# Optimization experiments

Measured on AMD Instinct MI355X. Metric: run time of the kernel, lower is better.

The kernel has to match this reference:

```python
import jax, jax.numpy as jnp
import numpy as np

VOCAB, EMBED, HID, LAYERS, OUT = 50000, 256, 256, 2, 50
B, S = 64, 512
H = HID // 2  # per-direction hidden size


def setup_inputs() -> dict:
    key = jax.random.key(0)
    ks = jax.random.split(key, 12)
    sc = 0.05
    embed = jax.random.normal(ks[0], (VOCAB, EMBED), jnp.float32) * sc
    embed = embed.at[1].set(0.0)  # padding_idx=1
    return {
        "x": jax.random.randint(ks[1], (B, S), 0, VOCAB),
        "embed": embed,
        "W1": jax.random.normal(ks[2], (HID, EMBED), jnp.float32) * sc,
        "b1": jax.random.normal(ks[3], (HID,), jnp.float32) * sc,
        "gru_Wih": jax.random.normal(ks[4], (LAYERS, 2, 3 * H, HID), jnp.float32) * sc,
        "gru_Whh": jax.random.normal(ks[5], (LAYERS, 2, 3 * H, H), jnp.float32) * sc,
        "gru_bih": jax.random.normal(ks[6], (LAYERS, 2, 3 * H), jnp.float32) * sc,
        "gru_bhh": jax.random.normal(ks[7], (LAYERS, 2, 3 * H), jnp.float32) * sc,
        "W2": jax.random.normal(ks[8], (HID, HID), jnp.float32) * sc,
        "b2": jax.random.normal(ks[9], (HID,), jnp.float32) * sc,
        "W3": jax.random.normal(ks[10], (OUT, HID), jnp.float32) * sc,
        "b3": jax.random.normal(ks[11], (OUT,), jnp.float32) * sc,
    }


def _gru_dir(x, Wih, Whh, bih, bhh, reverse):
    # x: [B, S, D]; PyTorch gate order: r, z, n. h0 = zeros.
    xp = jnp.einsum("bsd,gd->bsg", x, Wih) + bih  # [B, S, 3H], input proj hoisted out of scan
    xs = jnp.swapaxes(xp, 0, 1)  # [S, B, 3H]
    h0 = jnp.zeros((x.shape[0], Whh.shape[1]), x.dtype)

    def step(h, xt):
        hp = h @ Whh.T + bhh  # [B, 3H]
        xr, xz, xn = jnp.split(xt, 3, axis=-1)
        hr, hz, hn = jnp.split(hp, 3, axis=-1)
        r = jax.nn.sigmoid(xr + hr)
        z = jax.nn.sigmoid(xz + hz)
        n = jnp.tanh(xn + r * hn)
        h_new = (1.0 - z) * n + z * h
        return h_new, h_new

    _, ys = jax.lax.scan(step, h0, xs, reverse=reverse)  # outputs kept in original time order
    return jnp.swapaxes(ys, 0, 1)  # [B, S, H]


def reference(x, embed, W1, b1, gru_Wih, gru_Whh, gru_bih, gru_bhh, W2, b2, W3, b3):
    h = embed[x]  # [B, S, E]
    h = h @ W1.T + b1  # [B, S, HID]
    for l in range(gru_Wih.shape[0]):
        out_f = _gru_dir(h, gru_Wih[l, 0], gru_Whh[l, 0], gru_bih[l, 0], gru_bhh[l, 0], False)
        out_b = _gru_dir(h, gru_Wih[l, 1], gru_Whh[l, 1], gru_bih[l, 1], gru_bhh[l, 1], True)
        h = jnp.concatenate([out_f, out_b], axis=-1) + h  # bidirectional concat + residual
    h = jax.nn.gelu(h @ W2.T + b2, approximate=False)  # nn.GELU default is exact erf
    return h @ W3.T + b3  # [B, S, OUT]
```

## Files before the change

kernel.cpp:

```cpp
#include <hip/hip_runtime.h>

typedef unsigned int uint;
typedef unsigned short ushort;

typedef __attribute__((ext_vector_type(8))) short sh8;
typedef __attribute__((ext_vector_type(4))) float f32x4;

__device__ __forceinline__ ushort f2b(float f) {
    uint x = __float_as_uint(f);
    x += 0x7fffu + ((x >> 16) & 1u);
    return (ushort)(x >> 16);
}
__device__ __forceinline__ float b2f(ushort u) {
    return __uint_as_float(((uint)u) << 16);
}
__device__ __forceinline__ uint pack2(float a, float b) {
    return (uint)f2b(a) | ((uint)f2b(b) << 16);
}
__device__ __forceinline__ uint cvt_pk_bf16(float lo, float hi) {
    uint r;
    asm("v_cvt_pk_bf16_f32 %0, %1, %2" : "=v"(r) : "v"(lo), "v"(hi));
    return r;
}
__device__ __forceinline__ float frcp(float x) { return __builtin_amdgcn_rcpf(x); }
__device__ __forceinline__ float sigmf(float x) { return frcp(1.0f + __expf(-x)); }
__device__ __forceinline__ float tanhf2(float y) {
    return fmaf(2.0f, frcp(1.0f + __expf(-2.0f * y)), -1.0f);
}

__global__ __launch_bounds__(256) void k_detx(const uint* __restrict__ xw,
                                              int* __restrict__ flag) {
    __shared__ int sh[256];
    int t = threadIdx.x;
    int c = 0;
    for (int i = t; i < 2048; i += 256) c += (xw[2 * i + 1] == 0u) ? 1 : 0;
    sh[t] = c;
    __syncthreads();
    if (t == 0) {
        int s = 0;
        for (int i = 0; i < 256; i++) s += sh[i];
        flag[0] = (s >= 1843) ? 1 : 0;
    }
}

__global__ __launch_bounds__(256) void k_gather(const void* __restrict__ x,
                                                const float* __restrict__ embed,
                                                const int* __restrict__ flag,
                                                ushort* __restrict__ out) {
    int chunk = blockIdx.x * 256 + threadIdx.x;
    int row = chunk >> 5;
    int c = chunk & 31;
    int v;
    if (flag[0]) {
        v = (int)((const uint*)x)[2 * row];
    } else {
        v = ((const int*)x)[row];
    }
    v = min(max(v, 0), 49999);
    const float4* e = (const float4*)&embed[(size_t)v * 256 + (size_t)c * 8];
    float4 a = e[0], b = e[1];
    uint4 pv;
    pv.x = pack2(a.x, a.y);
    pv.y = pack2(a.z, a.w);
    pv.z = pack2(b.x, b.y);
    pv.w = pack2(b.z, b.w);
    *(uint4*)&out[(size_t)row * 256 + (size_t)c * 8] = pv;
}

__global__ __launch_bounds__(256) void k_gemm_bt(const ushort* __restrict__ A,
                                                 const float* __restrict__ Wf,
                                                 const float* __restrict__ bias,
                                                 ushort* __restrict__ Cb,
                                                 float* __restrict__ Cf,
                                                 int M, int N, int K, int gelu) {
    __shared__ __align__(16) ushort Al[128 * 32];
    __shared__ __align__(16) ushort Bl[128 * 32];
    int tid = threadIdx.x;
    int bm = blockIdx.x, bn = blockIdx.y;
    int wid = tid >> 6, lane = tid & 63;
    int ln = lane & 15, kq = lane >> 4;
    int wm = (wid & 1) * 64, wn = (wid >> 1) * 64;
    int rowA0 = bm * 128, rowB0 = bn * 128;

    f32x4 acc[4][4];
#pragma unroll
    for (int i = 0; i < 4; i++)
#pragma unroll
        for (int j = 0; j < 4; j++) acc[i][j] = (f32x4){0.f, 0.f, 0.f, 0.f};

    for (int kt = 0; kt < K; kt += 32) {
#pragma unroll
        for (int c = tid; c < 512; c += 256) {
            int r = c >> 2, c8 = (c & 3) * 8;
            *(uint4*)&Al[r * 32 + c8] =
                *(const uint4*)&A[(size_t)(rowA0 + r) * K + kt + c8];
            int nb = rowB0 + r;
            uint4 bv = {0u, 0u, 0u, 0u};
            if (nb < N) {
                const float4* wp = (const float4*)&Wf[(size_t)nb * K + kt + c8];
                float4 w0 = wp[0], w1 = wp[1];
                bv.x = pack2(w0.x, w0.y);
                bv.y = pack2(w0.z, w0.w);
                bv.z = pack2(w1.x, w1.y);
                bv.w = pack2(w1.z, w1.w);
            }
            *(uint4*)&Bl[r * 32 + c8] = bv;
        }
        __syncthreads();
        sh8 af[4], bfr[4];
#pragma unroll
        for (int i = 0; i < 4; i++)
            af[i] = *(const sh8*)&Al[(wm + i * 16 + ln) * 32 + kq * 8];
#pragma unroll
        for (int j = 0; j < 4; j++)
            bfr[j] = *(const sh8*)&Bl[(wn + j * 16 + ln) * 32 + kq * 8];
#pragma unroll
        for (int i = 0; i < 4; i++)
#pragma unroll
            for (int j = 0; j < 4; j++)
                acc[i][j] = __builtin_amdgcn_mfma_f32_16x16x32_bf16(
                    af[i], bfr[j], acc[i][j], 0, 0, 0);
        __syncthreads();
    }

#pragma unroll
    for (int i = 0; i < 4; i++)
#pragma unroll
        for (int j = 0; j < 4; j++) {
            int col = rowB0 + wn + j * 16 + ln;
            if (col >= N) continue;
            float bv = bias[col];
#pragma unroll
            for (int reg = 0; reg < 4; reg++) {
                int row = rowA0 + wm + i * 16 + kq * 4 + reg;
                float v = acc[i][j][reg] + bv;
                if (gelu) v = 0.5f * v * (1.0f + erff(v * 0.70710678118f));
                if (Cb) Cb[(size_t)row * N + col] = f2b(v);
                if (Cf) Cf[(size_t)row * N + col] = v;
            }
        }
}

struct PF {
    uint xr, xz, xn, rv;
};

#define GLOAD(dst, off, base, IMM)                                            \
    asm volatile("global_load_ushort %0, %1, %2 offset:" IMM                  \
                 : "=v"(dst)                                                  \
                 : "v"(off), "s"(base))

#define GSTORE(off, data, base)                                               \
    asm volatile("global_store_short %0, %1, %2" ::"v"(off), "v"(data),       \
                 "s"(base))

#define PREF(p)                                                               \
    {                                                                         \
        GLOAD(p.xr, xo_ld, xp, "0");                                          \
        GLOAD(p.xz, xo_ld, xp, "256");                                        \
        GLOAD(p.xn, xo_ld, xp, "512");                                        \
        GLOAD(p.rv, ho_ld, hb, "0");                                          \
        xo_ld += XS;                                                          \
        ho_ld += HS;                                                          \
    }

#define GSTEP(PAR, p, WN, DP)                                                 \
    {                                                                         \
        asm volatile("s_waitcnt vmcnt(" #WN ")");                             \
        __builtin_amdgcn_sched_barrier(0);                                    \
        float xr = __uint_as_float(p.xr << 16);                               \
        float xz = __uint_as_float(p.xz << 16);                               \
        float xn = __uint_as_float(p.xn << 16);                               \
        float rv = __uint_as_float(p.rv << 16);                               \
        if (DP) {                                                             \
            PREF(p)                                                           \
        }                                                                     \
        const ushort* hrd = lds + (PAR)*576 + (ln & 3) * 144 + kq * 8;        \
        sh8 a0 = *(const sh8*)(hrd);                                          \
        sh8 a1 = *(const sh8*)(hrd + 32);                                     \
        sh8 a2 = *(const sh8*)(hrd + 64);                                     \
        sh8 a3 = *(const sh8*)(hrd + 96);                                     \
        f32x4 accr = (f32x4){0.f, 0.f, 0.f, 0.f};                             \
        f32x4 accz = accr, accn = accr;                                       \
        accr = __builtin_amdgcn_mfma_f32_16x16x32_bf16(a0, bfrag[0][0], accr, 0, 0, 0); \
        accz = __builtin_amdgcn_mfma_f32_16x16x32_bf16(a0, bfrag[1][0], accz, 0, 0, 0); \
        accn = __builtin_amdgcn_mfma_f32_16x16x32_bf16(a0, bfrag[2][0], accn, 0, 0, 0); \
        accr = __builtin_amdgcn_mfma_f32_16x16x32_bf16(a1, bfrag[0][1], accr, 0, 0, 0); \
        accz = __builtin_amdgcn_mfma_f32_16x16x32_bf16(a1, bfrag[1][1], accz, 0, 0, 0); \
        accn = __builtin_amdgcn_mfma_f32_16x16x32_bf16(a1, bfrag[2][1], accn, 0, 0, 0); \
        accr = __builtin_amdgcn_mfma_f32_16x16x32_bf16(a2, bfrag[0][2], accr, 0, 0, 0); \
        accz = __builtin_amdgcn_mfma_f32_16x16x32_bf16(a2, bfrag[1][2], accz, 0, 0, 0); \
        accn = __builtin_amdgcn_mfma_f32_16x16x32_bf16(a2, bfrag[2][2], accn, 0, 0, 0); \
        accr = __builtin_amdgcn_mfma_f32_16x16x32_bf16(a3, bfrag[0][3], accr, 0, 0, 0); \
        accz = __builtin_amdgcn_mfma_f32_16x16x32_bf16(a3, bfrag[1][3], accz, 0, 0, 0); \
        accn = __builtin_amdgcn_mfma_f32_16x16x32_bf16(a3, bfrag[2][3], accn, 0, 0, 0); \
        float ar = b2 ? (b1 ? accr[3] : accr[2]) : (b1 ? accr[1] : accr[0]);  \
        float az = b2 ? (b1 ? accz[3] : accz[2]) : (b1 ? accz[1] : accz[0]);  \
        float an = b2 ? (b1 ? accn[3] : accn[2]) : (b1 ? accn[1] : accn[0]);  \
        float rg = sigmf(xr + ar + bh_r);                                     \
        float zg = sigmf(xz + az + bh_z);                                     \
        float ng = tanhf2(fmaf(rg, an + bh_n, xn));                           \
        float h = fmaf(zg, hstate - ng, ng);                                  \
        hstate = h;                                                           \
        float sv = h + rv;                                                    \
        uint pk = cvt_pk_bf16(h, sv);                                         \
        lds[(1 - (PAR)) * 576 + ob * 144 + jcol] = (ushort)pk;                \
        uint svb = pk >> 16;                                                  \
        GSTORE(ho_st, svb, hb);                                               \
        ho_st += HS;                                                          \
        asm volatile("s_waitcnt lgkmcnt(0)");                                 \
        __builtin_amdgcn_sched_barrier(0);                                    \
        __builtin_amdgcn_s_barrier();                                         \
        __builtin_amdgcn_sched_barrier(0);                                    \
    }

template <int DS>
__device__ __forceinline__ void gru_impl(const ushort* __restrict__ xp,
                                         const float* __restrict__ Whh_l,
                                         const float* __restrict__ bhh_l,
                                         ushort* __restrict__ hb,
                                         int dir, int b_base, int t,
                                         ushort* lds) {
    constexpr int XS = DS * 1536;
    constexpr int HS = DS * 512;
    const int w = t >> 6, l = t & 63;
    const int ln = l & 15, kq = l >> 4;
    const int jcol = (w << 4) + ln;
    const int ob = kq;
    const bool b1 = (ob & 1) != 0, b2 = (ob & 2) != 0;

    const float* Wd = Whh_l + (size_t)dir * 384 * 128;
    const float* bhh_d = bhh_l + dir * 384;

    sh8 bfrag[3][4];
#pragma unroll
    for (int g = 0; g < 3; g++)
#pragma unroll
        for (int kt = 0; kt < 4; kt++) {
            const float4* wp =
                (const float4*)(Wd + (size_t)(g * 128 + jcol) * 128 + kt * 32 + kq * 8);
            float4 w0 = wp[0], w1 = wp[1];
            uint4 pv;
            pv.x = pack2(w0.x, w0.y);
            pv.y = pack2(w0.z, w0.w);
            pv.z = pack2(w1.x, w1.y);
            pv.w = pack2(w1.z, w1.w);
            bfrag[g][kt] = *(sh8*)&pv;
        }

    const float bh_r = bhh_d[jcol];
    const float bh_z = bhh_d[128 + jcol];
    const float bh_n = bhh_d[256 + jcol];
    asm volatile("" ::"v"(bh_r), "v"(bh_z), "v"(bh_n));

    const int t0 = (DS > 0) ? 0 : 511;
    int row0 = (b_base + ob) * 512 + t0;
    int xo_ld = row0 * 1536 + (dir * 384 + jcol) * 2;
    int ho_ld = row0 * 512 + (dir * 128 + jcol) * 2;
    int ho_st = ho_ld;

    float hstate = 0.f;

    for (int i = t; i < 2 * 576; i += 512) lds[i] = 0;
    __syncthreads();

    PF pA, pB;
    PREF(pA)
    PREF(pB)

    GSTEP(0, pA, 4, 1)
    GSTEP(1, pB, 5, 1)
    for (int s = 2; s < 510; s += 2) {
        GSTEP(0, pA, 6, 1)
        GSTEP(1, pB, 6, 1)
    }
    GSTEP(0, pA, 6, 0)
    GSTEP(1, pB, 2, 0)
}

__global__ __launch_bounds__(512, 1) void k_gru(const ushort* __restrict__ xp,
                                                const float* __restrict__ Whh_l,
                                                const float* __restrict__ bhh_l,
                                                ushort* __restrict__ hb) {
    __shared__ __align__(16) ushort lds[2 * 576];
    const int dir = blockIdx.x & 1;
    const int b_base = (blockIdx.x >> 1) << 2;
    if (dir == 0)
        gru_impl<1>(xp, Whh_l, bhh_l, hb, dir, b_base, threadIdx.x, lds);
    else
        gru_impl<-1>(xp, Whh_l, bhh_l, hb, dir, b_base, threadIdx.x, lds);
}

extern "C" void kernel_launch(void* const* d_in, const int* in_sizes, int n_in,
                              void* d_out, int out_size, void* d_ws, size_t ws_size,
                              hipStream_t stream) {
    const void* x = d_in[0];
    const float* embed = (const float*)d_in[1];
    const float* W1 = (const float*)d_in[2];
    const float* b1 = (const float*)d_in[3];
    const float* Wih = (const float*)d_in[4];
    const float* Whh = (const float*)d_in[5];
    const float* bih = (const float*)d_in[6];
    const float* bhh = (const float*)d_in[7];
    const float* W2 = (const float*)d_in[8];
    const float* b2 = (const float*)d_in[9];
    const float* W3 = (const float*)d_in[10];
    const float* b3 = (const float*)d_in[11];

    char* ws = (char*)d_ws;
    ushort* xp = (ushort*)ws;
    ushort* hb = (ushort*)(ws + 32768ull * 768 * 2);
    ushort* embA = xp;
    ushort* g = xp;
    int* xflag = (int*)hb;

    k_detx<<<1, 256, 0, stream>>>((const uint*)x, xflag);
    k_gather<<<4096, 256, 0, stream>>>(x, embed, xflag, embA);
    k_gemm_bt<<<dim3(256, 2), 256, 0, stream>>>(embA, W1, b1, hb, (float*)0,
                                                32768, 256, 256, 0);

    k_gemm_bt<<<dim3(256, 6), 256, 0, stream>>>(hb, Wih, bih, xp, (float*)0,
                                                32768, 768, 256, 0);
    k_gru<<<32, 512, 0, stream>>>(xp, Whh, bhh, hb);

    k_gemm_bt<<<dim3(256, 6), 256, 0, stream>>>(hb, Wih + 196608, bih + 768,
                                                xp, (float*)0, 32768, 768, 256, 0);
    k_gru<<<32, 512, 0, stream>>>(xp, Whh + 98304, bhh + 768, hb);

    k_gemm_bt<<<dim3(256, 2), 256, 0, stream>>>(hb, W2, b2, g, (float*)0,
                                                32768, 256, 256, 1);
    k_gemm_bt<<<dim3(256, 1), 256, 0, stream>>>(g, W3, b3, (ushort*)0,
                                                (float*)d_out, 32768, 50, 256, 0);
}
```

Baseline: 674.0 us.

## Halve GRU block to 4 waves, each computing two 16-column hidden tiles

The recurrent GRU kernel now runs with 256 threads (4 waves) per block instead of 512. Each wave owns 32 hidden columns and issues 24 MFMAs per step instead of 12, with doubled prefetch registers, bias values and weight fragments. The aim is to cut the per-step block barrier cost and wave synchronization on the serial critical path, at the price of longer per-wave MFMA chains and higher register pressure.

After: 810.2 us. 20.2% more time.

```diff
diff --git a/kernel.cpp b/kernel.cpp
--- a/kernel.cpp
+++ b/kernel.cpp
@@ -142,7 +142,8 @@
 }
 
 struct PF {
-    uint xr, xz, xn, rv;
+    uint xr0, xz0, xn0, rv0;
+    uint xr1, xz1, xn1, rv1;
 };
 
 #define GLOAD(dst, off, base, IMM)                                            \
@@ -150,28 +151,38 @@
                  : "=v"(dst)                                                  \
                  : "v"(off), "s"(base))
 
-#define GSTORE(off, data, base)                                               \
-    asm volatile("global_store_short %0, %1, %2" ::"v"(off), "v"(data),       \
-                 "s"(base))
+#define GSTORE(off, data, base, IMM)                                          \
+    asm volatile("global_store_short %0, %1, %2 offset:" IMM ::"v"(off),      \
+                 "v"(data), "s"(base))
 
 #define PREF(p)                                                               \
     {                                                                         \
-        GLOAD(p.xr, xo_ld, xp, "0");                                          \
-        GLOAD(p.xz, xo_ld, xp, "256");                                        \
-        GLOAD(p.xn, xo_ld, xp, "512");                                        \
-        GLOAD(p.rv, ho_ld, hb, "0");                                          \
+        GLOAD(p.xr0, xo_ld, xp, "0");                                         \
+        GLOAD(p.xz0, xo_ld, xp, "256");                                       \
+        GLOAD(p.xn0, xo_ld, xp, "512");                                       \
+        GLOAD(p.rv0, ho_ld, hb, "0");                                         \
+        GLOAD(p.xr1, xo_ld, xp, "32");                                        \
+        GLOAD(p.xz1, xo_ld, xp, "288");                                       \
+        GLOAD(p.xn1, xo_ld, xp, "544");                                       \
+        GLOAD(p.rv1, ho_ld, hb, "32");                                        \
         xo_ld += XS;                                                          \
         ho_ld += HS;                                                          \
     }
+
+#define SEL(v) (b2 ? (b1 ? (v)[3] : (v)[2]) : (b1 ? (v)[1] : (v)[0]))
 
 #define GSTEP(PAR, p, WN, DP)                                                 \
     {                                                                         \
         asm volatile("s_waitcnt vmcnt(" #WN ")");                             \
         __builtin_amdgcn_sched_barrier(0);                                    \
-        float xr = __uint_as_float(p.xr << 16);                               \
-        float xz = __uint_as_float(p.xz << 16);                               \
-        float xn = __uint_as_float(p.xn << 16);                               \
-        float rv = __uint_as_float(p.rv << 16);                               \
+        float xr0 = __uint_as_float(p.xr0 << 16);                             \
+        float xz0 = __uint_as_float(p.xz0 << 16);                             \
+        float xn0 = __uint_as_float(p.xn0 << 16);                             \
+        float rv0 = __uint_as_float(p.rv0 << 16);                             \
+        float xr1 = __uint_as_float(p.xr1 << 16);                             \
+        float xz1 = __uint_as_float(p.xz1 << 16);                             \
+        float xn1 = __uint_as_float(p.xn1 << 16);                             \
+        float rv1 = __uint_as_float(p.rv1 << 16);                             \
         if (DP) {                                                             \
             PREF(p)                                                           \
         }                                                                     \
@@ -180,33 +191,53 @@
         sh8 a1 = *(const sh8*)(hrd + 32);                                     \
         sh8 a2 = *(const sh8*)(hrd + 64);                                     \
         sh8 a3 = *(const sh8*)(hrd + 96);                                     \
-        f32x4 accr = (f32x4){0.f, 0.f, 0.f, 0.f};                             \
-        f32x4 accz = accr, accn = accr;                                       \
-        accr = __builtin_amdgcn_mfma_f32_16x16x32_bf16(a0, bfrag[0][0], accr, 0, 0, 0); \
-        accz = __builtin_amdgcn_mfma_f32_16x16x32_bf16(a0, bfrag[1][0], accz, 0, 0, 0); \
-        accn = __builtin_amdgcn_mfma_f32_16x16x32_bf16(a0, bfrag[2][0], accn, 0, 0, 0); \
-        accr = __builtin_amdgcn_mfma_f32_16x16x32_bf16(a1, bfrag[0][1], accr, 0, 0, 0); \
-        accz = __builtin_amdgcn_mfma_f32_16x16x32_bf16(a1, bfrag[1][1], accz, 0, 0, 0); \
-        accn = __builtin_amdgcn_mfma_f32_16x16x32_bf16(a1, bfrag[2][1], accn, 0, 0, 0); \
-        accr = __builtin_amdgcn_mfma_f32_16x16x32_bf16(a2, bfrag[0][2], accr, 0, 0, 0); \
-        accz = __builtin_amdgcn_mfma_f32_16x16x32_bf16(a2, bfrag[1][2], accz, 0, 0, 0); \
-        accn = __builtin_amdgcn_mfma_f32_16x16x32_bf16(a2, bfrag[2][2], accn, 0, 0, 0); \
-        accr = __builtin_amdgcn_mfma_f32_16x16x32_bf16(a3, bfrag[0][3], accr, 0, 0, 0); \
-        accz = __builtin_amdgcn_mfma_f32_16x16x32_bf16(a3, bfrag[1][3], accz, 0, 0, 0); \
-        accn = __builtin_amdgcn_mfma_f32_16x16x32_bf16(a3, bfrag[2][3], accn, 0, 0, 0); \
-        float ar = b2 ? (b1 ? accr[3] : accr[2]) : (b1 ? accr[1] : accr[0]);  \
-        float az = b2 ? (b1 ? accz[3] : accz[2]) : (b1 ? accz[1] : accz[0]);  \
-        float an = b2 ? (b1 ? accn[3] : accn[2]) : (b1 ? accn[1] : accn[0]);  \
-        float rg = sigmf(xr + ar + bh_r);                                     \
-        float zg = sigmf(xz + az + bh_z);                                     \
-        float ng = tanhf2(fmaf(rg, an + bh_n, xn));                           \
-        float h = fmaf(zg, hstate - ng, ng);                                  \
-        hstate = h;                                                           \
-        float sv = h + rv;                                                    \
-        uint pk = cvt_pk_bf16(h, sv);                                         \
-        lds[(1 - (PAR)) * 576 + ob * 144 + jcol] = (ushort)pk;                \
-        uint svb = pk >> 16;                                                  \
-        GSTORE(ho_st, svb, hb);                                               \
+        f32x4 ac[6];                                                          \
+        _Pragma("unroll") for (int q_ = 0; q_ < 6; q_++)                      \
+            ac[q_] = (f32x4){0.f, 0.f, 0.f, 0.f};                             \
+        ac[0] = __builtin_amdgcn_mfma_f32_16x16x32_bf16(a0, bfrag[0][0], ac[0], 0, 0, 0); \
+        ac[1] = __builtin_amdgcn_mfma_f32_16x16x32_bf16(a0, bfrag[1][0], ac[1], 0, 0, 0); \
+        ac[2] = __builtin_amdgcn_mfma_f32_16x16x32_bf16(a0, bfrag[2][0], ac[2], 0, 0, 0); \
+        ac[3] = __builtin_amdgcn_mfma_f32_16x16x32_bf16(a0, bfrag[3][0], ac[3], 0, 0, 0); \
+        ac[4] = __builtin_amdgcn_mfma_f32_16x16x32_bf16(a0, bfrag[4][0], ac[4], 0, 0, 0); \
+        ac[5] = __builtin_amdgcn_mfma_f32_16x16x32_bf16(a0, bfrag[5][0], ac[5], 0, 0, 0); \
+        ac[0] = __builtin_amdgcn_mfma_f32_16x16x32_bf16(a1, bfrag[0][1], ac[0], 0, 0, 0); \
+        ac[1] = __builtin_amdgcn_mfma_f32_16x16x32_bf16(a1, bfrag[1][1], ac[1], 0, 0, 0); \
+        ac[2] = __builtin_amdgcn_mfma_f32_16x16x32_bf16(a1, bfrag[2][1], ac[2], 0, 0, 0); \
+        ac[3] = __builtin_amdgcn_mfma_f32_16x16x32_bf16(a1, bfrag[3][1], ac[3], 0, 0, 0); \
+        ac[4] = __builtin_amdgcn_mfma_f32_16x16x32_bf16(a1, bfrag[4][1], ac[4], 0, 0, 0); \
+        ac[5] = __builtin_amdgcn_mfma_f32_16x16x32_bf16(a1, bfrag[5][1], ac[5], 0, 0, 0); \
+        ac[0] = __builtin_amdgcn_mfma_f32_16x16x32_bf16(a2, bfrag[0][2], ac[0], 0, 0, 0); \
+        ac[1] = __builtin_amdgcn_mfma_f32_16x16x32_bf16(a2, bfrag[1][2], ac[1], 0, 0, 0); \
+        ac[2] = __builtin_amdgcn_mfma_f32_16x16x32_bf16(a2, bfrag[2][2], ac[2], 0, 0, 0); \
+        ac[3] = __builtin_amdgcn_mfma_f32_16x16x32_bf16(a2, bfrag[3][2], ac[3], 0, 0, 0); \
+        ac[4] = __builtin_amdgcn_mfma_f32_16x16x32_bf16(a2, bfrag[4][2], ac[4], 0, 0, 0); \
+        ac[5] = __builtin_amdgcn_mfma_f32_16x16x32_bf16(a2, bfrag[5][2], ac[5], 0, 0, 0); \
+        ac[0] = __builtin_amdgcn_mfma_f32_16x16x32_bf16(a3, bfrag[0][3], ac[0], 0, 0, 0); \
+        ac[1] = __builtin_amdgcn_mfma_f32_16x16x32_bf16(a3, bfrag[1][3], ac[1], 0, 0, 0); \
+        ac[2] = __builtin_amdgcn_mfma_f32_16x16x32_bf16(a3, bfrag[2][3], ac[2], 0, 0, 0); \
+        ac[3] = __builtin_amdgcn_mfma_f32_16x16x32_bf16(a3, bfrag[3][3], ac[3], 0, 0, 0); \
+        ac[4] = __builtin_amdgcn_mfma_f32_16x16x32_bf16(a3, bfrag[4][3], ac[4], 0, 0, 0); \
+        ac[5] = __builtin_amdgcn_mfma_f32_16x16x32_bf16(a3, bfrag[5][3], ac[5], 0, 0, 0); \
+        float ar0 = SEL(ac[0]), az0 = SEL(ac[1]), an0 = SEL(ac[2]);           \
+        float ar1 = SEL(ac[3]), az1 = SEL(ac[4]), an1 = SEL(ac[5]);           \
+        float rg0 = sigmf(xr0 + ar0 + bh_r0);                                 \
+        float zg0 = sigmf(xz0 + az0 + bh_z0);                                 \
+        float ng0 = tanhf2(fmaf(rg0, an0 + bh_n0, xn0));                      \
+        float h0 = fmaf(zg0, hst0 - ng0, ng0);                                \
+        hst0 = h0;                                                            \
+        float rg1 = sigmf(xr1 + ar1 + bh_r1);                                 \
+        float zg1 = sigmf(xz1 + az1 + bh_z1);                                 \
+        float ng1 = tanhf2(fmaf(rg1, an1 + bh_n1, xn1));                      \
+        float h1 = fmaf(zg1, hst1 - ng1, ng1);                                \
+        hst1 = h1;                                                            \
+        uint pk0 = cvt_pk_bf16(h0, h0 + rv0);                                 \
+        uint pk1 = cvt_pk_bf16(h1, h1 + rv1);                                 \
+        ushort* hw = lds + (1 - (PAR)) * 576 + kq * 144 + wb + ln;            \
+        hw[0] = (ushort)pk0;                                                  \
+        hw[16] = (ushort)pk1;                                                 \
+        uint sv0 = pk0 >> 16, sv1 = pk1 >> 16;                                \
+        GSTORE(ho_st, sv0, hb, "0");                                          \
+        GSTORE(ho_st, sv1, hb, "32");                                         \
         ho_st += HS;                                                          \
         asm volatile("s_waitcnt lgkmcnt(0)");                                 \
         __builtin_amdgcn_sched_barrier(0);                                    \
@@ -225,60 +256,66 @@
     constexpr int HS = DS * 512;
     const int w = t >> 6, l = t & 63;
     const int ln = l & 15, kq = l >> 4;
-    const int jcol = (w << 4) + ln;
-    const int ob = kq;
-    const bool b1 = (ob & 1) != 0, b2 = (ob & 2) != 0;
+    const int wb = w * 32;
+    const bool b1 = (kq & 1) != 0, b2 = (kq & 2) != 0;
 
     const float* Wd = Whh_l + (size_t)dir * 384 * 128;
     const float* bhh_d = bhh_l + dir * 384;
 
-    sh8 bfrag[3][4];
+    sh8 bfrag[6][4];
 #pragma unroll
     for (int g = 0; g < 3; g++)
 #pragma unroll
-        for (int kt = 0; kt < 4; kt++) {
-            const float4* wp =
-                (const float4*)(Wd + (size_t)(g * 128 + jcol) * 128 + kt * 32 + kq * 8);
-            float4 w0 = wp[0], w1 = wp[1];
-            uint4 pv;
-            pv.x = pack2(w0.x, w0.y);
-            pv.y = pack2(w0.z, w0.w);
-            pv.z = pack2(w1.x, w1.y);
-            pv.w = pack2(w1.z, w1.w);
-            bfrag[g][kt] = *(sh8*)&pv;
-        }
-
-    const float bh_r = bhh_d[jcol];
-    const float bh_z = bhh_d[128 + jcol];
-    const float bh_n = bhh_d[256 + jcol];
-    asm volatile("" ::"v"(bh_r), "v"(bh_z), "v"(bh_n));
+        for (int c = 0; c < 2; c++)
+#pragma unroll
+            for (int kt = 0; kt < 4; kt++) {
+                const float4* wp = (const float4*)(
+                    Wd + (size_t)(g * 128 + wb + c * 16 + ln) * 128 + kt * 32 +
+                    kq * 8);
+                float4 w0 = wp[0], w1 = wp[1];
+                uint4 pv;
+                pv.x = pack2(w0.x, w0.y);
+                pv.y = pack2(w0.z, w0.w);
+                pv.z = pack2(w1.x, w1.y);
+                pv.w = pack2(w1.z, w1.w);
+                bfrag[c * 3 + g][kt] = *(sh8*)&pv;
+            }
+
+    const float bh_r0 = bhh_d[wb + ln];
+    const float bh_z0 = bhh_d[128 + wb + ln];
+    const float bh_n0 = bhh_d[256 + wb + ln];
+    const float bh_r1 = bhh_d[wb + 16 + ln];
+    const float bh_z1 = bhh_d[128 + wb + 16 + ln];
+    const float bh_n1 = bhh_d[256 + wb + 16 + ln];
+    asm volatile("" ::"v"(bh_r0), "v"(bh_z0), "v"(bh_n0), "v"(bh_r1),
+                 "v"(bh_z1), "v"(bh_n1));
 
     const int t0 = (DS > 0) ? 0 : 511;
-    int row0 = (b_base + ob) * 512 + t0;
-    int xo_ld = row0 * 1536 + (dir * 384 + jcol) * 2;
-    int ho_ld = row0 * 512 + (dir * 128 + jcol) * 2;
+    int row0 = (b_base + kq) * 512 + t0;
+    int xo_ld = row0 * 1536 + (dir * 384 + wb + ln) * 2;
+    int ho_ld = row0 * 512 + (dir * 128 + wb + ln) * 2;
     int ho_st = ho_ld;
 
-    float hstate = 0.f;
-
-    for (int i = t; i < 2 * 576; i += 512) lds[i] = 0;
+    float hst0 = 0.f, hst1 = 0.f;
+
+    for (int i = t; i < 2 * 576; i += 256) lds[i] = 0;
     __syncthreads();
 
     PF pA, pB;
     PREF(pA)
     PREF(pB)
 
-    GSTEP(0, pA, 4, 1)
-    GSTEP(1, pB, 5, 1)
+    GSTEP(0, pA, 8, 1)
+    GSTEP(1, pB, 10, 1)
     for (int s = 2; s < 510; s += 2) {
-        GSTEP(0, pA, 6, 1)
-        GSTEP(1, pB, 6, 1)
-    }
-    GSTEP(0, pA, 6, 0)
-    GSTEP(1, pB, 2, 0)
-}
-
-__global__ __launch_bounds__(512, 1) void k_gru(const ushort* __restrict__ xp,
+        GSTEP(0, pA, 12, 1)
+        GSTEP(1, pB, 12, 1)
+    }
+    GSTEP(0, pA, 12, 0)
+    GSTEP(1, pB, 4, 0)
+}
+
+__global__ __launch_bounds__(256, 1) void k_gru(const ushort* __restrict__ xp,
                                                 const float* __restrict__ Whh_l,
                                                 const float* __restrict__ bhh_l,
                                                 ushort* __restrict__ hb) {
@@ -321,11 +358,11 @@
 
     k_gemm_bt<<<dim3(256, 6), 256, 0, stream>>>(hb, Wih, bih, xp, (float*)0,
                                                 32768, 768, 256, 0);
-    k_gru<<<32, 512, 0, stream>>>(xp, Whh, bhh, hb);
+    k_gru<<<32, 256, 0, stream>>>(xp, Whh, bhh, hb);
 
     k_gemm_bt<<<dim3(256, 6), 256, 0, stream>>>(hb, Wih + 196608, bih + 768,
                                                 xp, (float*)0, 32768, 768, 256, 0);
-    k_gru<<<32, 512, 0, stream>>>(xp, Whh + 98304, bhh + 768, hb);
+    k_gru<<<32, 256, 0, stream>>>(xp, Whh + 98304, bhh + 768, hb);
 
     k_gemm_bt<<<dim3(256, 2), 256, 0, stream>>>(hb, W2, b2, g, (float*)0,
                                                 32768, 256, 256, 1);
```
